# Performance work log

Hardware: AMD Instinct MI355X
Metric: run time of the kernel (lower is better)

## Reference

```python
import jax, jax.numpy as jnp
import numpy as np

B, PP, LP, H = 128, 1024, 128, 256  # graphs, protein atoms/graph, ligand atoms/graph, hidden
NP, NL = B * PP, B * LP


def setup_inputs() -> dict:
    key = jax.random.key(0)
    ks = jax.random.split(key, 16)
    s = 0.02
    return {
        "protein_pos": 10.0 * jax.random.normal(ks[0], (NP, 3), jnp.float32),
        "ligand_pos": 10.0 * jax.random.normal(ks[1], (NL, 3), jnp.float32),
        "protein_element": jax.random.randint(ks[2], (NP,), 0, 128),
        "protein_aa": jax.random.randint(ks[3], (NP,), 0, 32),
        "protein_is_backbone": jax.random.randint(ks[4], (NP,), 0, 2),
        "ligand_type": jax.random.randint(ks[5], (NL,), 0, 16),
        "protein_batch": jnp.repeat(jnp.arange(B), PP),  # block-contiguous segments
        "ligand_batch": jnp.repeat(jnp.arange(B), LP),
        "E_elem": s * jax.random.normal(ks[6], (128, H), jnp.float32),
        "E_aa": s * jax.random.normal(ks[7], (32, H), jnp.float32),
        "E_bb": s * jax.random.normal(ks[8], (2, H), jnp.float32),
        "E_lig": s * jax.random.normal(ks[9], (16, H), jnp.float32),
        "Wd1": s * jax.random.normal(ks[10], (H, H), jnp.float32),
        "bd1": jnp.zeros((H,), jnp.float32),
        "Wd2": s * jax.random.normal(ks[11], (H, H), jnp.float32),
        "bd2": jnp.zeros((H,), jnp.float32),
        "Wa1": s * jax.random.normal(ks[12], (2 * H + 2, H), jnp.float32),
        "ba1": jnp.zeros((H,), jnp.float32),
        "Wa2": s * jax.random.normal(ks[13], (H, 1), jnp.float32),
        "ba2": jnp.zeros((1,), jnp.float32),
    }


def _pool_by_batch(x, batch, bsz):
    # mean-pool rows of x into bsz segments (index_add_ + bincount in torch)
    summed = jax.ops.segment_sum(x, batch, num_segments=bsz)
    counts = jax.ops.segment_sum(jnp.ones((x.shape[0],), x.dtype), batch, num_segments=bsz)
    return summed / jnp.maximum(counts, 1.0)[:, None]


def reference(protein_pos, ligand_pos, protein_element, protein_aa, protein_is_backbone,
              ligand_type, protein_batch, ligand_batch,
              E_elem, E_aa, E_bb, E_lig, Wd1, bd1, Wd2, bd2, Wa1, ba1, Wa2, ba2):
    # protein / ligand node embeddings
    h_protein = E_elem[protein_element] + E_aa[protein_aa] + E_bb[protein_is_backbone]
    h_ligand = E_lig[ligand_type]

    # compose_context: protein first, then ligand (mask_ligand = [0]*NP + [1]*NL)
    h_ctx = jnp.concatenate([h_protein, h_ligand], axis=0)

    # stub denoiser: pointwise 2-layer SiLU MLP producing out['h']
    h_out = jax.nn.silu(h_ctx @ Wd1 + bd1) @ Wd2 + bd2
    protein_h = h_out[:protein_pos.shape[0]]
    ligand_h = h_out[protein_pos.shape[0]:]

    pooled_protein = _pool_by_batch(protein_h, protein_batch, B)  # [B, H]
    pooled_ligand = _pool_by_batch(ligand_h, ligand_batch, B)     # [B, H]

    # contact features: per-graph cdist(lig, prot), min over protein atoms,
    # then mean & min over ligand atoms. Uniform block layout -> dense reshape.
    prot = protein_pos.reshape(B, PP, 3)
    lig = ligand_pos.reshape(B, LP, 3)
    d2 = jnp.sum((lig[:, :, None, :] - prot[:, None, :, :]) ** 2, axis=-1)  # [B, LP, PP]
    dist = jnp.sqrt(d2)
    min_lp = dist.min(axis=2)                                    # [B, LP]
    contact = jnp.stack([min_lp.mean(axis=1), min_lp.min(axis=1)], axis=-1)  # [B, 2]

    graph_feat = jnp.concatenate([pooled_protein, pooled_ligand, contact], axis=-1)  # [B, 2H+2]
    affinity = (jax.nn.silu(graph_feat @ Wa1 + ba1) @ Wa2 + ba2).squeeze(-1)  # [B]
    return affinity
```

## Files before the change

### kernel.cpp

```cpp
#include <hip/hip_runtime.h>
#include <hip/hip_bf16.h>

typedef _Float16 f16;
typedef _Float16 h2 __attribute__((ext_vector_type(2)));

#define B_   128
#define PP_  1024
#define LP_  128
#define H_   256


__global__ void __launch_bounds__(256) prep_k(
    const float* __restrict__ W1,
    const float* __restrict__ Ee, const float* __restrict__ Ea,
    const float* __restrict__ Eb, const float* __restrict__ El,
    const float* __restrict__ bd1,
    const float* __restrict__ ppos, const float* __restrict__ lpos,
    f16* __restrict__ tbl, float* __restrict__ cbuf)
{
  __shared__ float px[4 * 264], py[4 * 264], pz[4 * 264];
  __shared__ float lmin[128];
  __shared__ float src[256];
  const int bid = blockIdx.x, tid = threadIdx.x;

  if (bid < 178) {
    const float* s;
    float badd = 0.f;
    if (bid < 128)      s = Ee + bid * 256;
    else if (bid < 160) s = Ea + (bid - 128) * 256;
    else if (bid < 162) { s = Eb + (bid - 160) * 256; badd = bd1[tid]; }
    else                { s = El + (bid - 162) * 256; badd = bd1[tid]; }
    src[tid] = s[tid];
    __syncthreads();
    float a0 = 0.f, a1 = 0.f, a2 = 0.f, a3 = 0.f;
#pragma unroll 4
    for (int k = 0; k < 256; k += 4) {
      a0 += src[k]     * W1[(k)     * 256 + tid];
      a1 += src[k + 1] * W1[(k + 1) * 256 + tid];
      a2 += src[k + 2] * W1[(k + 2) * 256 + tid];
      a3 += src[k + 3] * W1[(k + 3) * 256 + tid];
    }
    tbl[bid * 256 + tid] = (f16)(((a0 + a1) + (a2 + a3)) + badd);
    return;
  }

  const int b = bid - 178;
#pragma unroll
  for (int r = 0; r < 4; ++r) {
    const int i = r * 256 + tid;
    const int d = (i >> 8) * 264 + (i & 255);
    const float* p = ppos + ((size_t)b * PP_ + i) * 3;
    px[d] = p[0]; py[d] = p[1]; pz[d] = p[2];
  }
  __syncthreads();
  {
    const int lig = tid >> 1, prt = tid & 1;
    const float* lp = lpos + ((size_t)b * LP_ + lig) * 3;
    const float lx = lp[0], ly = lp[1], lz = lp[2];
    float m = 3.4e38f;
#pragma unroll 1
    for (int s2 = prt * 2; s2 < prt * 2 + 2; ++s2) {
      const float4* X4 = (const float4*)(px + s2 * 264);
      const float4* Y4 = (const float4*)(py + s2 * 264);
      const float4* Z4 = (const float4*)(pz + s2 * 264);
#pragma unroll 4
      for (int i = 0; i < 64; ++i) {
        float4 X = X4[i], Y = Y4[i], Z = Z4[i];
        float dx, dy, dz, d2;
        dx = lx - X.x; dy = ly - Y.x; dz = lz - Z.x;
        d2 = dx * dx + dy * dy + dz * dz; m = fminf(m, d2);
        dx = lx - X.y; dy = ly - Y.y; dz = lz - Z.y;
        d2 = dx * dx + dy * dy + dz * dz; m = fminf(m, d2);
        dx = lx - X.z; dy = ly - Y.z; dz = lz - Z.z;
        d2 = dx * dx + dy * dy + dz * dz; m = fminf(m, d2);
        dx = lx - X.w; dy = ly - Y.w; dz = lz - Z.w;
        d2 = dx * dx + dy * dy + dz * dz; m = fminf(m, d2);
      }
    }
    m = fminf(m, __shfl_xor(m, 1));
    if (prt == 0) lmin[lig] = sqrtf(m);
  }
  __syncthreads();
  if (tid < 64) {
    const float a0 = lmin[tid], a1 = lmin[tid + 64];
    float sm = a0 + a1, mn = fminf(a0, a1);
#pragma unroll
    for (int off = 32; off; off >>= 1) {
      sm += __shfl_down(sm, off);
      mn = fminf(mn, __shfl_down(mn, off));
    }
    if (tid == 0) {
      cbuf[b * 2 + 0] = sm * (1.f / (float)LP_);
      cbuf[b * 2 + 1] = mn;
    }
  }
}

__global__ void __launch_bounds__(1024) pool_head_k(
    const int* __restrict__ pel, const int* __restrict__ paa,
    const int* __restrict__ pbb, const int* __restrict__ ltyp,
    const f16* __restrict__ tbl, const float* __restrict__ cbuf,
    const float* __restrict__ W2, const float* __restrict__ bd2,
    const float* __restrict__ Wa1, const float* __restrict__ ba1,
    const float* __restrict__ Wa2, const float* __restrict__ ba2,
    float* __restrict__ out)
{
  __shared__ float redP[8][256];
  __shared__ float redL[8][256];
  __shared__ float ys[512];
  __shared__ float pooled[512];
  __shared__ float part[512];
  __shared__ float red[4];
  const int b = blockIdx.x, tid = threadIdx.x;
  const int c2 = tid & 127;
  const int rg = tid >> 7;

  float aP0 = 0.f, aP1 = 0.f, aL0 = 0.f, aL1 = 0.f;
  {
    const int pbase = b * PP_ + rg * 128;
#pragma unroll 4
    for (int r = 0; r < 128; ++r) {
      const int idx = pbase + r;
      h2 va = *(const h2*)(tbl + pel[idx] * 256 + c2 * 2);
      h2 vb = *(const h2*)(tbl + 32768 + paa[idx] * 256 + c2 * 2);
      h2 vc = *(const h2*)(tbl + 40960 + pbb[idx] * 256 + c2 * 2);
      h2 s = va + vb + vc;
      float p0 = (float)s[0], p1 = (float)s[1];
      aP0 += p0 * __builtin_amdgcn_rcpf(1.f + __expf(-p0));
      aP1 += p1 * __builtin_amdgcn_rcpf(1.f + __expf(-p1));
    }
    const int lbase = b * LP_ + rg * 16;
#pragma unroll 4
    for (int r = 0; r < 16; ++r) {
      h2 v = *(const h2*)(tbl + 41472 + ltyp[lbase + r] * 256 + c2 * 2);
      float p0 = (float)v[0], p1 = (float)v[1];
      aL0 += p0 * __builtin_amdgcn_rcpf(1.f + __expf(-p0));
      aL1 += p1 * __builtin_amdgcn_rcpf(1.f + __expf(-p1));
    }
  }
  redP[rg][c2 * 2] = aP0; redP[rg][c2 * 2 + 1] = aP1;
  redL[rg][c2 * 2] = aL0; redL[rg][c2 * 2 + 1] = aL1;
  __syncthreads();

  if (tid < 512) {
    const int h = tid >> 8, c = tid & 255;
    float s = 0.f;
    if (h == 0) {
#pragma unroll
      for (int g = 0; g < 8; ++g) s += redP[g][c];
    } else {
#pragma unroll
      for (int g = 0; g < 8; ++g) s += redL[g][c];
    }
    ys[h * 256 + c] = s;
  }
  __syncthreads();

  if (tid < 512) {
    const int h = tid >> 8, n = tid & 255;
    const float* y = ys + h * 256;
    float a0 = 0.f, a1 = 0.f, a2 = 0.f, a3 = 0.f;
#pragma unroll 4
    for (int k = 0; k < 256; k += 4) {
      a0 += y[k]     * W2[(k)     * 256 + n];
      a1 += y[k + 1] * W2[(k + 1) * 256 + n];
      a2 += y[k + 2] * W2[(k + 2) * 256 + n];
      a3 += y[k + 3] * W2[(k + 3) * 256 + n];
    }
    const float scale = h ? (1.f / (float)LP_) : (1.f / (float)PP_);
    pooled[tid] = ((a0 + a1) + (a2 + a3)) * scale + bd2[n];
  }
  __syncthreads();

  if (tid < 512) {
    const int kh = tid >> 8, j = tid & 255;
    const float* W = Wa1 + kh * 256 * 256 + j;
    const float* p = pooled + kh * 256;
    float a0 = 0.f, a1 = 0.f, a2 = 0.f, a3 = 0.f;
#pragma unroll 4
    for (int n = 0; n < 256; n += 4) {
      a0 += p[n]     * W[(n)     * 256];
      a1 += p[n + 1] * W[(n + 1) * 256];
      a2 += p[n + 2] * W[(n + 2) * 256];
      a3 += p[n + 3] * W[(n + 3) * 256];
    }
    part[tid] = (a0 + a1) + (a2 + a3);
  }
  __syncthreads();

  if (tid < 256) {
    const float c0 = cbuf[b * 2], c1 = cbuf[b * 2 + 1];
    float pre = part[tid] + part[256 + tid] + ba1[tid]
              + c0 * Wa1[512 * 256 + tid] + c1 * Wa1[513 * 256 + tid];
    float si = pre * __builtin_amdgcn_rcpf(1.f + __expf(-pre));
    float p = si * Wa2[tid];
#pragma unroll
    for (int off = 32; off; off >>= 1) p += __shfl_down(p, off);
    if ((tid & 63) == 0) red[tid >> 6] = p;
  }
  __syncthreads();
  if (tid == 0) out[b] = (red[0] + red[1]) + (red[2] + red[3]) + ba2[0];
}

extern "C" void kernel_launch(void* const* d_in, const int* in_sizes, int n_in,
                              void* d_out, int out_size, void* d_ws, size_t ws_size,
                              hipStream_t stream)
{
  const float* protein_pos = (const float*)d_in[0];
  const float* ligand_pos  = (const float*)d_in[1];
  const int*   pel  = (const int*)d_in[2];
  const int*   paa  = (const int*)d_in[3];
  const int*   pbb  = (const int*)d_in[4];
  const int*   ltyp = (const int*)d_in[5];
  const float* Ee  = (const float*)d_in[8];
  const float* Ea  = (const float*)d_in[9];
  const float* Eb  = (const float*)d_in[10];
  const float* El  = (const float*)d_in[11];
  const float* Wd1 = (const float*)d_in[12];
  const float* bd1 = (const float*)d_in[13];
  const float* Wd2 = (const float*)d_in[14];
  const float* bd2 = (const float*)d_in[15];
  const float* Wa1 = (const float*)d_in[16];
  const float* ba1 = (const float*)d_in[17];
  const float* Wa2 = (const float*)d_in[18];
  const float* ba2 = (const float*)d_in[19];
  float* out = (float*)d_out;

  char* ws = (char*)d_ws;
  f16*   tbl  = (f16*)(ws);
  float* cbuf = (float*)(ws + 98304);

  prep_k<<<306, 256, 0, stream>>>(Wd1, Ee, Ea, Eb, El, bd1,
                                  protein_pos, ligand_pos, tbl, cbuf);
  pool_head_k<<<B_, 1024, 0, stream>>>(pel, paa, pbb, ltyp, tbl, cbuf,
                                       Wd2, bd2, Wa1, ba1, Wa2, ba2, out);
}
```

Measured before the change: 150.8 us.

## Split pooling into many-block gather kernel with atomics and separate head kernel

The fused pool+head kernel, which ran only 128 blocks, is split in two. A gather/SiLU pooling kernel runs 1152 blocks of 256 threads, uses vectorized index loads and h4 table reads, and combines partial sums with global atomics into a workspace that prep_k zeroes. A separate head kernel then does the two matvecs, with the K dimension split over all 1024 threads for more parallelism. The aim is to fill the GPU during the gather-heavy pooling phase, at the cost of an extra kernel launch, atomic traffic, and non-deterministic summation order.

```diff
diff --git a/kernel.cpp b/kernel.cpp
--- a/kernel.cpp
+++ b/kernel.cpp
@@ -2,7 +2,7 @@
 #include <hip/hip_bf16.h>
 
 typedef _Float16 f16;
-typedef _Float16 h2 __attribute__((ext_vector_type(2)));
+typedef _Float16 h4 __attribute__((ext_vector_type(4)));
 
 #define B_   128
 #define PP_  1024
@@ -16,12 +16,13 @@
     const float* __restrict__ Eb, const float* __restrict__ El,
     const float* __restrict__ bd1,
     const float* __restrict__ ppos, const float* __restrict__ lpos,
-    f16* __restrict__ tbl, float* __restrict__ cbuf)
+    f16* __restrict__ tbl, float* __restrict__ cbuf, float* __restrict__ ysum)
 {
   __shared__ float px[4 * 264], py[4 * 264], pz[4 * 264];
   __shared__ float lmin[128];
   __shared__ float src[256];
   const int bid = blockIdx.x, tid = threadIdx.x;
+  if (bid < 256) ysum[bid * 256 + tid] = 0.f;
 
   if (bid < 178) {
     const float* s;
@@ -96,102 +97,130 @@
   }
 }
 
-__global__ void __launch_bounds__(1024) pool_head_k(
+__global__ void __launch_bounds__(256, 4) gpool_k(
     const int* __restrict__ pel, const int* __restrict__ paa,
     const int* __restrict__ pbb, const int* __restrict__ ltyp,
-    const f16* __restrict__ tbl, const float* __restrict__ cbuf,
+    const f16* __restrict__ tbl, float* __restrict__ ysum)
+{
+  const int tid = threadIdx.x;
+  const int wave = __builtin_amdgcn_readfirstlane(tid >> 6);
+  const int lane = tid & 63;
+  const int batch = blockIdx.x / 9, g = blockIdx.x % 9;
+  const int c0 = lane * 4;
+  float acc[4] = {0.f, 0.f, 0.f, 0.f};
+
+  if (g < 8) {
+    const int base = batch * PP_ + g * 128 + wave * 32;
+#pragma unroll
+    for (int ch = 0; ch < 4; ++ch) {
+      const int cb = base + ch * 8;
+      const int4 e0 = *(const int4*)(pel + cb), e1 = *(const int4*)(pel + cb + 4);
+      const int4 a0 = *(const int4*)(paa + cb), a1 = *(const int4*)(paa + cb + 4);
+      const int4 b0 = *(const int4*)(pbb + cb), b1 = *(const int4*)(pbb + cb + 4);
+      const int el[8] = {e0.x, e0.y, e0.z, e0.w, e1.x, e1.y, e1.z, e1.w};
+      const int aa[8] = {a0.x, a0.y, a0.z, a0.w, a1.x, a1.y, a1.z, a1.w};
+      const int bb[8] = {b0.x, b0.y, b0.z, b0.w, b1.x, b1.y, b1.z, b1.w};
+      h4 s[8];
+#pragma unroll
+      for (int r = 0; r < 8; ++r) {
+        h4 va = *(const h4*)(tbl + el[r] * 256 + c0);
+        h4 vb = *(const h4*)(tbl + 32768 + aa[r] * 256 + c0);
+        h4 vc = *(const h4*)(tbl + 40960 + bb[r] * 256 + c0);
+        s[r] = (va + vb) + vc;
+      }
+#pragma unroll
+      for (int r = 0; r < 8; ++r)
+#pragma unroll
+        for (int i = 0; i < 4; ++i) {
+          float pre = (float)s[r][i];
+          acc[i] += pre * __builtin_amdgcn_rcpf(1.f + __expf(-pre));
+        }
+    }
+    float* pool = ysum + batch * 256 + c0;
+#pragma unroll
+    for (int i = 0; i < 4; ++i) atomicAdd(pool + i, acc[i]);
+  } else {
+    const int base = batch * LP_ + wave * 32;
+#pragma unroll
+    for (int ch = 0; ch < 4; ++ch) {
+      const int cb = base + ch * 8;
+      const int4 l0 = *(const int4*)(ltyp + cb), l1 = *(const int4*)(ltyp + cb + 4);
+      const int lt[8] = {l0.x, l0.y, l0.z, l0.w, l1.x, l1.y, l1.z, l1.w};
+      h4 s[8];
+#pragma unroll
+      for (int r = 0; r < 8; ++r)
+        s[r] = *(const h4*)(tbl + 41472 + lt[r] * 256 + c0);
+#pragma unroll
+      for (int r = 0; r < 8; ++r)
+#pragma unroll
+        for (int i = 0; i < 4; ++i) {
+          float pre = (float)s[r][i];
+          acc[i] += pre * __builtin_amdgcn_rcpf(1.f + __expf(-pre));
+        }
+    }
+    float* pool = ysum + 32768 + batch * 256 + c0;
+#pragma unroll
+    for (int i = 0; i < 4; ++i) atomicAdd(pool + i, acc[i]);
+  }
+}
+
+__global__ void __launch_bounds__(1024) head_k(
+    const float* __restrict__ ysum, const float* __restrict__ cbuf,
     const float* __restrict__ W2, const float* __restrict__ bd2,
     const float* __restrict__ Wa1, const float* __restrict__ ba1,
     const float* __restrict__ Wa2, const float* __restrict__ ba2,
     float* __restrict__ out)
 {
-  __shared__ float redP[8][256];
-  __shared__ float redL[8][256];
-  __shared__ float ys[512];
-  __shared__ float pooled[512];
-  __shared__ float part[512];
-  __shared__ float red[4];
+  __shared__ float ys[512], pooled[512], p2[1024], part[1024], red[4];
   const int b = blockIdx.x, tid = threadIdx.x;
-  const int c2 = tid & 127;
-  const int rg = tid >> 7;
-
-  float aP0 = 0.f, aP1 = 0.f, aL0 = 0.f, aL1 = 0.f;
+
+  if (tid < 512)
+    ys[tid] = (tid < 256) ? ysum[b * 256 + tid]
+                          : ysum[32768 + b * 256 + (tid - 256)];
+  __syncthreads();
+
   {
-    const int pbase = b * PP_ + rg * 128;
-#pragma unroll 4
-    for (int r = 0; r < 128; ++r) {
-      const int idx = pbase + r;
-      h2 va = *(const h2*)(tbl + pel[idx] * 256 + c2 * 2);
-      h2 vb = *(const h2*)(tbl + 32768 + paa[idx] * 256 + c2 * 2);
-      h2 vc = *(const h2*)(tbl + 40960 + pbb[idx] * 256 + c2 * 2);
-      h2 s = va + vb + vc;
-      float p0 = (float)s[0], p1 = (float)s[1];
-      aP0 += p0 * __builtin_amdgcn_rcpf(1.f + __expf(-p0));
-      aP1 += p1 * __builtin_amdgcn_rcpf(1.f + __expf(-p1));
-    }
-    const int lbase = b * LP_ + rg * 16;
-#pragma unroll 4
-    for (int r = 0; r < 16; ++r) {
-      h2 v = *(const h2*)(tbl + 41472 + ltyp[lbase + r] * 256 + c2 * 2);
-      float p0 = (float)v[0], p1 = (float)v[1];
-      aL0 += p0 * __builtin_amdgcn_rcpf(1.f + __expf(-p0));
-      aL1 += p1 * __builtin_amdgcn_rcpf(1.f + __expf(-p1));
-    }
-  }
-  redP[rg][c2 * 2] = aP0; redP[rg][c2 * 2 + 1] = aP1;
-  redL[rg][c2 * 2] = aL0; redL[rg][c2 * 2 + 1] = aL1;
-  __syncthreads();
-
-  if (tid < 512) {
-    const int h = tid >> 8, c = tid & 255;
-    float s = 0.f;
-    if (h == 0) {
-#pragma unroll
-      for (int g = 0; g < 8; ++g) s += redP[g][c];
-    } else {
-#pragma unroll
-      for (int g = 0; g < 8; ++g) s += redL[g][c];
-    }
-    ys[h * 256 + c] = s;
-  }
-  __syncthreads();
-
+    const int kh2 = tid >> 9, h = (tid >> 8) & 1, n = tid & 255;
+    const float* y = ys + h * 256 + kh2 * 128;
+    const float* W = W2 + kh2 * 128 * 256 + n;
+    float a[8];
+#pragma unroll
+    for (int u = 0; u < 8; ++u) a[u] = 0.f;
+#pragma unroll 2
+    for (int k = 0; k < 128; k += 8)
+#pragma unroll
+      for (int u = 0; u < 8; ++u)
+        a[u] += y[k + u] * W[(k + u) * 256];
+    p2[tid] = ((a[0] + a[1]) + (a[2] + a[3])) + ((a[4] + a[5]) + (a[6] + a[7]));
+  }
+  __syncthreads();
   if (tid < 512) {
     const int h = tid >> 8, n = tid & 255;
-    const float* y = ys + h * 256;
-    float a0 = 0.f, a1 = 0.f, a2 = 0.f, a3 = 0.f;
-#pragma unroll 4
-    for (int k = 0; k < 256; k += 4) {
-      a0 += y[k]     * W2[(k)     * 256 + n];
-      a1 += y[k + 1] * W2[(k + 1) * 256 + n];
-      a2 += y[k + 2] * W2[(k + 2) * 256 + n];
-      a3 += y[k + 3] * W2[(k + 3) * 256 + n];
-    }
     const float scale = h ? (1.f / (float)LP_) : (1.f / (float)PP_);
-    pooled[tid] = ((a0 + a1) + (a2 + a3)) * scale + bd2[n];
-  }
-  __syncthreads();
-
-  if (tid < 512) {
-    const int kh = tid >> 8, j = tid & 255;
-    const float* W = Wa1 + kh * 256 * 256 + j;
-    const float* p = pooled + kh * 256;
-    float a0 = 0.f, a1 = 0.f, a2 = 0.f, a3 = 0.f;
-#pragma unroll 4
-    for (int n = 0; n < 256; n += 4) {
-      a0 += p[n]     * W[(n)     * 256];
-      a1 += p[n + 1] * W[(n + 1) * 256];
-      a2 += p[n + 2] * W[(n + 2) * 256];
-      a3 += p[n + 3] * W[(n + 3) * 256];
-    }
-    part[tid] = (a0 + a1) + (a2 + a3);
+    pooled[tid] = (p2[tid] + p2[512 + tid]) * scale + bd2[n];
+  }
+  __syncthreads();
+
+  {
+    const int kq = tid >> 8, j = tid & 255;
+    const float* p = pooled + kq * 128;
+    const float* W = Wa1 + kq * 128 * 256 + j;
+    float a[8];
+#pragma unroll
+    for (int u = 0; u < 8; ++u) a[u] = 0.f;
+#pragma unroll 2
+    for (int n = 0; n < 128; n += 8)
+#pragma unroll
+      for (int u = 0; u < 8; ++u)
+        a[u] += p[n + u] * W[(n + u) * 256];
+    part[tid] = ((a[0] + a[1]) + (a[2] + a[3])) + ((a[4] + a[5]) + (a[6] + a[7]));
   }
   __syncthreads();
 
   if (tid < 256) {
     const float c0 = cbuf[b * 2], c1 = cbuf[b * 2 + 1];
-    float pre = part[tid] + part[256 + tid] + ba1[tid]
-              + c0 * Wa1[512 * 256 + tid] + c1 * Wa1[513 * 256 + tid];
+    float pre = (part[tid] + part[256 + tid]) + (part[512 + tid] + part[768 + tid])
+              + ba1[tid] + c0 * Wa1[512 * 256 + tid] + c1 * Wa1[513 * 256 + tid];
     float si = pre * __builtin_amdgcn_rcpf(1.f + __expf(-pre));
     float p = si * Wa2[tid];
 #pragma unroll
@@ -229,9 +258,10 @@
   char* ws = (char*)d_ws;
   f16*   tbl  = (f16*)(ws);
   float* cbuf = (float*)(ws + 98304);
+  float* ysum = (float*)(ws + 102400);
 
   prep_k<<<306, 256, 0, stream>>>(Wd1, Ee, Ea, Eb, El, bd1,
-                                  protein_pos, ligand_pos, tbl, cbuf);
-  pool_head_k<<<B_, 1024, 0, stream>>>(pel, paa, pbb, ltyp, tbl, cbuf,
-                                       Wd2, bd2, Wa1, ba1, Wa2, ba2, out);
-}
+                                  protein_pos, ligand_pos, tbl, cbuf, ysum);
+  gpool_k<<<B_ * 9, 256, 0, stream>>>(pel, paa, pbb, ltyp, tbl, ysum);
+  head_k<<<B_, 1024, 0, stream>>>(ysum, cbuf, Wd2, bd2, Wa1, ba1, Wa2, ba2, out);
+}
```

New measurement: 141.3 us. 1.07x faster.
